# Kernel tuning notes

Measured on AMD Instinct MI355X. Metric: run time of the kernel, lower is better.

## Reference

```python
import jax, jax.numpy as jnp
import numpy as np

NEG_SLOPE = 0.2  # PyG GATConv default negative_slope
HEADS1, HID = 8, 256


def gat_conv(x, src, dst, W, att_src, att_dst, bias, heads, out_ch):
    """PyG-style GATConv: project, per-edge attention, segment softmax over dst, scatter-add."""
    N = x.shape[0]
    h = (x @ W.T).reshape(N, heads, out_ch)                 # [N,H,C]
    a_s = jnp.einsum('nhc,hc->nh', h, att_src)              # [N,H]
    a_d = jnp.einsum('nhc,hc->nh', h, att_dst)
    e = jax.nn.leaky_relu(a_s[src] + a_d[dst], NEG_SLOPE)   # [E,H]
    m = jax.ops.segment_max(e, dst, num_segments=N)         # stable softmax per dst node
    ex = jnp.exp(e - m[dst])
    denom = jax.ops.segment_sum(ex, dst, num_segments=N)
    alpha = ex / (denom[dst] + 1e-16)                       # [E,H]
    out = jax.ops.segment_sum(alpha[:, :, None] * h[src], dst, num_segments=N)  # [N,H,C]
    return out.reshape(N, heads * out_ch) + bias


def setup_inputs() -> dict:
    key = jax.random.key(0)
    ks = jax.random.split(key, 20)
    Nc, Ncol, E = 4000, 16000, 100000
    nf, cf, gain, hid, H, emb = 64, 128, 2, HID, HEADS1, 128
    s = 0.05
    return {
        'constraints_state': jax.random.normal(ks[0], (Nc, nf), jnp.float32),
        'columns_state':     jax.random.normal(ks[1], (Ncol, cf), jnp.float32),
        'edges':             jax.random.randint(ks[2], (2, E), 0, Nc + Ncol, jnp.int64),
        'W_node': jax.random.normal(ks[3], (hid, nf * gain), jnp.float32) * s,
        'b_node': jnp.zeros((hid,), jnp.float32),
        'W_col':  jax.random.normal(ks[4], (hid, cf * gain), jnp.float32) * s,
        'b_col':  jnp.zeros((hid,), jnp.float32),
        'W1':       jax.random.normal(ks[5], (H * hid, hid), jnp.float32) * s,
        'att_src1': jax.random.normal(ks[6], (H, hid), jnp.float32) * s,
        'att_dst1': jax.random.normal(ks[7], (H, hid), jnp.float32) * s,
        'b1':       jnp.zeros((H * hid,), jnp.float32),
        'W2':       jax.random.normal(ks[8], (hid, H * hid), jnp.float32) * s,
        'att_src2': jax.random.normal(ks[9], (1, hid), jnp.float32) * s,
        'att_dst2': jax.random.normal(ks[10], (1, hid), jnp.float32) * s,
        'b2':       jnp.zeros((hid,), jnp.float32),
        'W_out': jax.random.normal(ks[11], (emb, hid), jnp.float32) * s,
        'b_out': jnp.zeros((emb,), jnp.float32),
    }


def reference(constraints_state, columns_state, edges,
              W_node, b_node, W_col, b_col,
              W1, att_src1, att_dst1, b1,
              W2, att_src2, att_dst2, b2,
              W_out, b_out):
    gain = 2
    x_n = jnp.tile(constraints_state, (1, gain))
    x_c = jnp.tile(columns_state, (1, gain))
    h_n = jax.nn.relu(x_n @ W_node.T + b_node)
    h_c = jax.nn.relu(x_c @ W_col.T + b_col)
    x = jnp.concatenate([h_n, h_c], axis=0)                 # [N, hid]
    N = x.shape[0]
    loops = jnp.arange(N)
    # conv1: edges as given (+ self-loops, PyG default)
    src1 = jnp.concatenate([edges[0], loops])
    dst1 = jnp.concatenate([edges[1], loops])
    x = jax.nn.relu(gat_conv(x, src1, dst1, W1, att_src1, att_dst1, b1, HEADS1, HID))
    # conv2: flipped edges (+ self-loops), 1 head
    src2 = jnp.concatenate([edges[1], loops])
    dst2 = jnp.concatenate([edges[0], loops])
    x = jax.nn.relu(gat_conv(x, src2, dst2, W2, att_src2, att_dst2, b2, 1, HID))
    logits = x[-columns_state.shape[0]:] @ W_out.T + b_out  # [Ncol, embed_dim]
    return logits
```

## Files before the change

kernel.cpp:

```cpp
#include <hip/hip_runtime.h>


#define NEG_SLOPE 0.2f

typedef __attribute__((ext_vector_type(8))) short bf16x8;
typedef __attribute__((ext_vector_type(4))) float f32x4;

__device__ __forceinline__ float bf2f(unsigned short u) {
  return __uint_as_float(((unsigned)u) << 16);
}
__device__ __forceinline__ unsigned short f2bf(float f) {
  unsigned u = __float_as_uint(f);
  u += 0x7fffu + ((u >> 16) & 1u);
  return (unsigned short)(u >> 16);
}

__device__ __forceinline__ void async_copy16(const void* g, void* l) {
  __builtin_amdgcn_global_load_lds(
      (const __attribute__((address_space(1))) unsigned int*)g,
      (__attribute__((address_space(3))) unsigned int*)l, 16, 0, 0);
}

__global__ void prep(const float* __restrict__ Wn, const float* __restrict__ Wc,
                     const float* __restrict__ W1, const float* __restrict__ W2,
                     const float* __restrict__ Wout,
                     const float* __restrict__ cons, const float* __restrict__ cols,
                     const float* __restrict__ att_s1, const float* __restrict__ att_d1,
                     unsigned short* __restrict__ Wn_b, unsigned short* __restrict__ Wc_b,
                     unsigned short* __restrict__ W1b, unsigned short* __restrict__ W2b,
                     unsigned short* __restrict__ Woutb,
                     unsigned short* __restrict__ consb, unsigned short* __restrict__ colsb,
                     float* __restrict__ v_s1, float* __restrict__ v_d1,
                     int n_cons, int n_cols) {
  const int S0 = 256 * 64;
  const int S1 = 256 * 128;
  const int S2 = 2048 * 256;
  const int S3 = 256 * 2048;
  const int S4 = 128 * 256;
  const int S5 = 2048;
  int total = S0 + S1 + S2 + S3 + S4 + n_cons + n_cols + S5;
  for (int idx = blockIdx.x * 256 + threadIdx.x; idx < total; idx += gridDim.x * 256) {
    int i = idx;
    if (i < S0) { int o = i >> 6, j = i & 63;
      Wn_b[i] = f2bf(Wn[o * 128 + j] + Wn[o * 128 + 64 + j]); continue; }
    i -= S0;
    if (i < S1) { int o = i >> 7, j = i & 127;
      Wc_b[i] = f2bf(Wc[o * 256 + j] + Wc[o * 256 + 128 + j]); continue; }
    i -= S1;
    if (i < S2) { W1b[i] = f2bf(W1[i]); continue; }
    i -= S2;
    if (i < S3) { W2b[i] = f2bf(W2[i]); continue; }
    i -= S3;
    if (i < S4) { Woutb[i] = f2bf(Wout[i]); continue; }
    i -= S4;
    if (i < n_cons) { consb[i] = f2bf(cons[i]); continue; }
    i -= n_cons;
    if (i < n_cols) { colsb[i] = f2bf(cols[i]); continue; }
    i -= n_cols;
    {
      int h = i >> 8, k = i & 255;
      const float* Wrow = W1 + (size_t)h * 256 * 256 + k;
      const float* as = att_s1 + h * 256;
      const float* ad = att_d1 + h * 256;
      float s = 0.f, d = 0.f;
      for (int c = 0; c < 256; ++c) {
        float w = Wrow[(size_t)c * 256];
        s += as[c] * w;
        d += ad[c] * w;
      }
      v_s1[i] = s; v_d1[i] = d;
    }
  }
}

__global__ __launch_bounds__(256) void a1_dots(const unsigned short* __restrict__ xb,
                                               const float* __restrict__ v_s,
                                               const float* __restrict__ v_d,
                                               float* __restrict__ a_s,
                                               float* __restrict__ a_d, int N) {
  __shared__ float vs[2048], vd[2048];
  for (int i = threadIdx.x; i < 2048; i += 256) { vs[i] = v_s[i]; vd[i] = v_d[i]; }
  __syncthreads();
  int n = blockIdx.x * 256 + threadIdx.x;
  if (n >= N) return;
  const unsigned short* row = xb + (size_t)n * 256;
  float s[8] = {}, d[8] = {};
  for (int c = 0; c < 256; c += 8) {
    bf16x8 xv = *(const bf16x8*)(row + c);
    float xf[8];
#pragma unroll
    for (int i = 0; i < 8; ++i) xf[i] = bf2f(((const unsigned short*)&xv)[i]);
#pragma unroll
    for (int h = 0; h < 8; ++h)
#pragma unroll
      for (int i = 0; i < 8; ++i) {
        s[h] += xf[i] * vs[h * 256 + c + i];
        d[h] += xf[i] * vd[h * 256 + c + i];
      }
  }
#pragma unroll
  for (int h = 0; h < 8; ++h) { a_s[n * 8 + h] = s[h]; a_d[n * 8 + h] = d[h]; }
}

__global__ __launch_bounds__(256) void a2_dots(const unsigned short* __restrict__ h2,
                                               const float* __restrict__ att_s,
                                               const float* __restrict__ att_d,
                                               float* __restrict__ a_s,
                                               float* __restrict__ a_d, int N) {
  __shared__ float ss[256], sd[256];
  if (threadIdx.x < 256) {
    ss[threadIdx.x] = att_s[threadIdx.x];
    sd[threadIdx.x] = att_d[threadIdx.x];
  }
  __syncthreads();
  int n = blockIdx.x * 256 + threadIdx.x;
  if (n >= N) return;
  const unsigned short* row = h2 + (size_t)n * 256;
  float s = 0.f, d = 0.f;
  for (int c = 0; c < 256; c += 8) {
    bf16x8 xv = *(const bf16x8*)(row + c);
#pragma unroll
    for (int i = 0; i < 8; ++i) {
      float hv = bf2f(((const unsigned short*)&xv)[i]);
      s += hv * ss[c + i];
      d += hv * sd[c + i];
    }
  }
  a_s[n] = s;
  a_d[n] = d;
}

template <bool C_BF16, bool BIAS, bool RELU, bool BDIAG>
__global__ __launch_bounds__(512) void gemm_mfma_bt(const unsigned short* __restrict__ A,
                                                    const unsigned short* __restrict__ W,
                                                    const float* __restrict__ bias,
                                                    void* __restrict__ Cv,
                                                    int M, int K, int Nout, int lda) {
  __shared__ short smem[2 * 128 * 64];
  short* sA = smem;
  short* sB = smem + 128 * 64;
  float* Cf = (float*)Cv;
  unsigned short* Cb = (unsigned short*)Cv;

  const int tid = threadIdx.x;
  const int lane = tid & 63, w = tid >> 6;

  const int gx = gridDim.x;
  const int nwg = gx * gridDim.y;
  int orig = blockIdx.y * gx + blockIdx.x;
  int q = nwg >> 3, r = nwg & 7;
  int xcd = orig & 7, idx = orig >> 3;
  int wg = (xcd < r ? xcd * (q + 1) : r * (q + 1) + (xcd - r) * q) + idx;
  const int m0 = (wg / gx) * 128, n0 = (wg % gx) * 128;

  const int koff = BDIAG ? (n0 >> 8) << 8 : 0;
  const int wm = (w & 3) * 32, wn = (w >> 2) * 64;
  const int fr = lane & 15;
  const int frs = fr & 7;
  const int quad = lane >> 4;

  f32x4 acc[2][4];
#pragma unroll
  for (int i = 0; i < 2; ++i)
#pragma unroll
    for (int j = 0; j < 4; ++j) acc[i][j] = (f32x4){0.f, 0.f, 0.f, 0.f};

  for (int k0 = 0; k0 < K; k0 += 64) {
#pragma unroll
    for (int i = 0; i < 2; ++i) {
      int c = i * 512 + tid;
      int row = c >> 3, kc = c & 7;
      int kcs = kc ^ (row & 7);
      int grow = m0 + row;
      if (grow >= M) grow = M - 1;
      async_copy16(A + (size_t)grow * lda + koff + k0 + kcs * 8, &sA[(i * 512 + w * 64) * 8]);
    }
#pragma unroll
    for (int i = 0; i < 2; ++i) {
      int c = i * 512 + tid;
      int row = c >> 3, kc = c & 7;
      int kcs = kc ^ (row & 7);
      async_copy16(W + (size_t)(n0 + row) * K + k0 + kcs * 8, &sB[(i * 512 + w * 64) * 8]);
    }
    __syncthreads();

#pragma unroll
    for (int ks = 0; ks < 2; ++ks) {
      bf16x8 af[2], bfr[4];
#pragma unroll
      for (int mi = 0; mi < 2; ++mi) {
        int row = wm + mi * 16 + fr;
        af[mi] = *(const bf16x8*)&sA[(row * 8 + ((ks * 4 + quad) ^ frs)) * 8];
      }
#pragma unroll
      for (int ni = 0; ni < 4; ++ni) {
        int row = wn + ni * 16 + fr;
        bfr[ni] = *(const bf16x8*)&sB[(row * 8 + ((ks * 4 + quad) ^ frs)) * 8];
      }
#pragma unroll
      for (int mi = 0; mi < 2; ++mi)
#pragma unroll
        for (int ni = 0; ni < 4; ++ni)
          acc[mi][ni] = __builtin_amdgcn_mfma_f32_16x16x32_bf16(
              af[mi], bfr[ni], acc[mi][ni], 0, 0, 0);
    }
    __syncthreads();
  }

  if (C_BF16) {
    unsigned short* hsh = (unsigned short*)smem;
#pragma unroll
    for (int mi = 0; mi < 2; ++mi)
#pragma unroll
      for (int ni = 0; ni < 4; ++ni) {
        int col = wn + ni * 16 + fr;
        float bv = BIAS ? bias[n0 + col] : 0.f;
        f32x4 v = acc[mi][ni];
#pragma unroll
        for (int r = 0; r < 4; ++r) {
          int row = wm + mi * 16 + quad * 4 + r;
          float x = v[r] + bv;
          if (RELU) x = fmaxf(x, 0.f);
          hsh[row * 128 + (col ^ (((row >> 2) & 3) << 5))] = f2bf(x);
        }
      }
    __syncthreads();
#pragma unroll
    for (int i = 0; i < 4; ++i) {
      int slot = i * 512 + tid;
      int row = slot >> 4, cg = slot & 15;
      int colbase = cg * 8;
      bf16x8 val = *(const bf16x8*)&hsh[row * 128 + (colbase ^ (((row >> 2) & 3) << 5))];
      int grow = m0 + row;
      if (grow < M)
        *(bf16x8*)(Cb + (size_t)grow * Nout + n0 + colbase) = val;
    }
  } else {
#pragma unroll
    for (int mi = 0; mi < 2; ++mi)
#pragma unroll
      for (int ni = 0; ni < 4; ++ni) {
        int col = n0 + wn + ni * 16 + fr;
        float bv = BIAS ? bias[col] : 0.f;
        f32x4 v = acc[mi][ni];
#pragma unroll
        for (int r = 0; r < 4; ++r) {
          int row = m0 + wm + mi * 16 + quad * 4 + r;
          if (row < M) {
            float x = v[r] + bv;
            if (RELU) x = fmaxf(x, 0.f);
            Cf[(size_t)row * Nout + col] = x;
          }
        }
      }
  }
}

__global__ void build_count(const void* __restrict__ edges_raw, int E, int N,
                            int* __restrict__ esrc, int* __restrict__ edst,
                            int* __restrict__ cnt1, int* __restrict__ cnt2, int E1) {
  const long long* p64 = (const long long*)edges_raw;
  const int* p32 = (const int*)edges_raw;
  bool is64 = true;
#pragma unroll
  for (int i = 0; i < 8; ++i) {
    long long v = p64[i];
    if (v < 0 || v >= N) is64 = false;
  }
  int idx = blockIdx.x * 256 + threadIdx.x;
  if (idx >= E1) return;
  int s, d;
  if (idx < E) {
    if (is64) { s = (int)p64[idx]; d = (int)p64[E + idx]; }
    else      { s = p32[idx];      d = p32[E + idx]; }
  } else {
    s = d = idx - E;
  }
  esrc[idx] = s;
  edst[idx] = d;
  atomicAdd(&cnt1[d], 1);
  atomicAdd(&cnt2[s], 1);
}

__device__ __forceinline__ void scan_one(const int* __restrict__ cnt,
                                         int* __restrict__ indptr,
                                         int* __restrict__ cur, int N, int* buf) {
  int t = threadIdx.x, lane = t & 63, w = t >> 6;
  int running = 0;
  for (int base = 0; base < N; base += 1024) {
    int v = (base + t < N) ? cnt[base + t] : 0;
    int incl = v;
#pragma unroll
    for (int off = 1; off < 64; off <<= 1) {
      int y = __shfl_up(incl, off);
      if (lane >= off) incl += y;
    }
    if (lane == 63) buf[w] = incl;
    __syncthreads();
    if (t < 16) {
      int x = buf[t];
#pragma unroll
      for (int off = 1; off < 16; off <<= 1) {
        int y = __shfl_up(x, off);
        if (t >= off) x += y;
      }
      buf[t] = x;
    }
    __syncthreads();
    int woff = w ? buf[w - 1] : 0;
    int tot = buf[15];
    if (base + t < N) {
      int excl = running + woff + incl - v;
      indptr[base + t] = excl;
      cur[base + t] = excl;
    }
    running += tot;
    __syncthreads();
  }
  if (t == 0) indptr[N] = running;
  __syncthreads();
}

__global__ __launch_bounds__(1024) void scan2_kernel(const int* cnt1, int* indptr1, int* cur1,
                                                     const int* cnt2, int* indptr2, int* cur2,
                                                     int N) {
  __shared__ int buf[16];
  scan_one(cnt1, indptr1, cur1, N, buf);
  scan_one(cnt2, indptr2, cur2, N, buf);
}

__global__ void scatter_edges(const int* __restrict__ esrc, const int* __restrict__ edst,
                              int* __restrict__ cur1, int* __restrict__ cur2,
                              int* __restrict__ nbr1, int* __restrict__ nbr2, int E1) {
  int e = blockIdx.x * 256 + threadIdx.x;
  if (e >= E1) return;
  int s = esrc[e], d = edst[e];
  int p1 = atomicAdd(&cur1[d], 1);
  nbr1[p1] = s;
  int p2 = atomicAdd(&cur2[s], 1);
  nbr2[p2] = d;
}

__global__ __launch_bounds__(256) void alpha1_kernel(const float* __restrict__ a_s,
                                                     const float* __restrict__ a_d,
                                                     const int* __restrict__ indptr,
                                                     const int* __restrict__ nbr,
                                                     float* __restrict__ alpha, int N) {
  int n = blockIdx.x * 256 + threadIdx.x;
  if (n >= N) return;
  int start = indptr[n], end = indptr[n + 1];
  float ad[8];
  *(float4*)&ad[0] = *(const float4*)&a_d[n * 8];
  *(float4*)&ad[4] = *(const float4*)&a_d[n * 8 + 4];
  float m[8], ssum[8];
#pragma unroll
  for (int h = 0; h < 8; ++h) { m[h] = -1e30f; ssum[h] = 0.f; }
  for (int p = start; p < end; ++p) {
    int s = nbr[p];
    float as[8];
    *(float4*)&as[0] = *(const float4*)&a_s[s * 8];
    *(float4*)&as[4] = *(const float4*)&a_s[s * 8 + 4];
#pragma unroll
    for (int h = 0; h < 8; ++h) {
      float e = as[h] + ad[h];
      e = e > 0.f ? e : NEG_SLOPE * e;
      float nm = fmaxf(m[h], e);
      ssum[h] = ssum[h] * __expf(m[h] - nm) + __expf(e - nm);
      m[h] = nm;
    }
  }
  float inv[8];
#pragma unroll
  for (int h = 0; h < 8; ++h) inv[h] = 1.f / (ssum[h] + 1e-16f);
  for (int p = start; p < end; ++p) {
    int s = nbr[p];
    float as[8];
    *(float4*)&as[0] = *(const float4*)&a_s[s * 8];
    *(float4*)&as[4] = *(const float4*)&a_s[s * 8 + 4];
    float av[8];
#pragma unroll
    for (int h = 0; h < 8; ++h) {
      float e = as[h] + ad[h];
      e = e > 0.f ? e : NEG_SLOPE * e;
      av[h] = __expf(e - m[h]) * inv[h];
    }
    *(float4*)&alpha[(size_t)p * 8] = *(const float4*)&av[0];
    *(float4*)&alpha[(size_t)p * 8 + 4] = *(const float4*)&av[4];
  }
}

__global__ __launch_bounds__(256) void agg1_kernel(const unsigned short* __restrict__ xb,
                                                   const float* __restrict__ alpha,
                                                   const int* __restrict__ indptr,
                                                   const int* __restrict__ nbr,
                                                   unsigned short* __restrict__ agg,
                                                   int N) {
  __shared__ float al_sh[4][64 * 8];
  const int w = threadIdx.x >> 6, lane = threadIdx.x & 63;
  const int dst = blockIdx.x * 4 + w;
  if (dst >= N) return;
  const int start = indptr[dst];
  const int deg = indptr[dst + 1] - start;
  const int c0 = lane * 4;

  float acc[8][4];
#pragma unroll
  for (int h = 0; h < 8; ++h)
#pragma unroll
    for (int i = 0; i < 4; ++i) acc[h][i] = 0.f;

  for (int base = 0; base < deg; base += 64) {
    int cnt = min(64, deg - base);
    int s = 0;
    if (lane < cnt) {
      int slot = start + base + lane;
      s = nbr[slot];
      f32x4 a0 = *(const f32x4*)&alpha[(size_t)slot * 8];
      f32x4 a1 = *(const f32x4*)&alpha[(size_t)slot * 8 + 4];
      *(f32x4*)&al_sh[w][lane * 8] = a0;
      *(f32x4*)&al_sh[w][lane * 8 + 4] = a1;
    }
    __builtin_amdgcn_wave_barrier();
    for (int j = 0; j < cnt; ++j) {
      int sj = __shfl(s, j);
      f32x4 alo = *(const f32x4*)&al_sh[w][j * 8];
      f32x4 ahi = *(const f32x4*)&al_sh[w][j * 8 + 4];
      ushort4 xv = *(const ushort4*)(xb + (size_t)sj * 256 + c0);
      float x0 = bf2f(xv.x), x1 = bf2f(xv.y), x2 = bf2f(xv.z), x3 = bf2f(xv.w);
#pragma unroll
      for (int h = 0; h < 4; ++h) {
        acc[h][0] += alo[h] * x0; acc[h][1] += alo[h] * x1;
        acc[h][2] += alo[h] * x2; acc[h][3] += alo[h] * x3;
      }
#pragma unroll
      for (int h = 0; h < 4; ++h) {
        acc[h + 4][0] += ahi[h] * x0; acc[h + 4][1] += ahi[h] * x1;
        acc[h + 4][2] += ahi[h] * x2; acc[h + 4][3] += ahi[h] * x3;
      }
    }
    __builtin_amdgcn_wave_barrier();
  }

  unsigned short* op = agg + (size_t)dst * 2048;
#pragma unroll
  for (int h = 0; h < 8; ++h) {
    unsigned short ov[4];
#pragma unroll
    for (int i = 0; i < 4; ++i) ov[i] = f2bf(acc[h][i]);
    *((ushort4*)(op + h * 256 + c0)) = *((const ushort4*)ov);
  }
}

__global__ __launch_bounds__(256) void agg2_fused(const unsigned short* __restrict__ h2,
                                                  const float* __restrict__ a_s,
                                                  const float* __restrict__ a_d,
                                                  const int* __restrict__ indptr,
                                                  const int* __restrict__ nbr,
                                                  const float* __restrict__ b2,
                                                  unsigned short* __restrict__ x3,
                                                  int Nc, int Ncol) {
  const int w = threadIdx.x >> 6, lane = threadIdx.x & 63;
  const int i0 = blockIdx.x * 4 + w;
  if (i0 >= Ncol) return;
  const int dst = Nc + i0;
  const int start = indptr[dst];
  const int deg = indptr[dst + 1] - start;
  const float ad = a_d[dst];
  float run_m = -1e30f, run_s = 0.f;
  float acc[4] = {0.f, 0.f, 0.f, 0.f};
  const int c0 = lane * 4;

  for (int base = 0; base < deg; base += 64) {
    int cnt = min(64, deg - base);
    float ev = -1e30f;
    int s = 0;
    if (lane < cnt) {
      s = nbr[start + base + lane];
      float e = a_s[s] + ad;
      ev = e > 0.f ? e : NEG_SLOPE * e;
    }
    float cm = ev;
#pragma unroll
    for (int off = 32; off; off >>= 1) cm = fmaxf(cm, __shfl_xor(cm, off));
    float nm = fmaxf(run_m, cm);
    float sc = __expf(run_m - nm);
    float e = (lane < cnt) ? __expf(ev - nm) : 0.f;
    float cs = e;
#pragma unroll
    for (int off = 32; off; off >>= 1) cs += __shfl_xor(cs, off);
    run_s = run_s * sc + cs;
    run_m = nm;
#pragma unroll
    for (int i = 0; i < 4; ++i) acc[i] *= sc;
    for (int j = 0; j < cnt; ++j) {
      int sj = __shfl(s, j);
      float al = __shfl(e, j);
      ushort4 hv = *(const ushort4*)(h2 + (size_t)sj * 256 + c0);
      acc[0] += al * bf2f(hv.x);
      acc[1] += al * bf2f(hv.y);
      acc[2] += al * bf2f(hv.z);
      acc[3] += al * bf2f(hv.w);
    }
  }

  float inv = 1.f / (run_s + 1e-16f);
  float4 bv = *(const float4*)&b2[c0];
  unsigned short ov[4];
  ov[0] = f2bf(fmaxf(acc[0] * inv + bv.x, 0.f));
  ov[1] = f2bf(fmaxf(acc[1] * inv + bv.y, 0.f));
  ov[2] = f2bf(fmaxf(acc[2] * inv + bv.z, 0.f));
  ov[3] = f2bf(fmaxf(acc[3] * inv + bv.w, 0.f));
  *((ushort4*)(x3 + (size_t)i0 * 256 + c0)) = *((const ushort4*)ov);
}

extern "C" void kernel_launch(void* const* d_in, const int* in_sizes, int n_in,
                              void* d_out, int out_size, void* d_ws, size_t ws_size,
                              hipStream_t stream) {
  (void)n_in; (void)out_size; (void)ws_size;
  const float* constraints = (const float*)d_in[0];
  const float* columns     = (const float*)d_in[1];
  const void*  edges       = d_in[2];
  const float* W_node = (const float*)d_in[3];
  const float* b_node = (const float*)d_in[4];
  const float* W_col  = (const float*)d_in[5];
  const float* b_col  = (const float*)d_in[6];
  const float* W1       = (const float*)d_in[7];
  const float* att_src1 = (const float*)d_in[8];
  const float* att_dst1 = (const float*)d_in[9];
  const float* b1       = (const float*)d_in[10];
  const float* W2       = (const float*)d_in[11];
  const float* att_src2 = (const float*)d_in[12];
  const float* att_dst2 = (const float*)d_in[13];
  const float* b2       = (const float*)d_in[14];
  const float* W_out    = (const float*)d_in[15];
  const float* b_out    = (const float*)d_in[16];

  const int Nc   = in_sizes[0] / 64;
  const int Ncol = in_sizes[1] / 128;
  const int E    = in_sizes[2] / 2;
  const int N    = Nc + Ncol;
  const int E1   = E + N;

  char* p = (char*)d_ws;
  size_t off = 0;
  auto alloc = [&](size_t nbytes) -> void* {
    void* r = p + off;
    off = (off + nbytes + 255) & ~(size_t)255;
    return r;
  };
  unsigned short* Wn_b  = (unsigned short*)alloc(2ull * 256 * 64);
  unsigned short* Wc_b  = (unsigned short*)alloc(2ull * 256 * 128);
  unsigned short* W1b   = (unsigned short*)alloc(2ull * 2048 * 256);
  unsigned short* W2b   = (unsigned short*)alloc(2ull * 256 * 2048);
  unsigned short* Woutb = (unsigned short*)alloc(2ull * 128 * 256);
  unsigned short* consb = (unsigned short*)alloc(2ull * (size_t)Nc * 64);
  unsigned short* colsb = (unsigned short*)alloc(2ull * (size_t)Ncol * 128);
  unsigned short* xb    = (unsigned short*)alloc(2ull * (size_t)N * 256);
  float* v_s1 = (float*)alloc(sizeof(float) * 8 * 256);
  float* v_d1 = (float*)alloc(sizeof(float) * 8 * 256);
  float* a_s1 = (float*)alloc(sizeof(float) * (size_t)N * 8);
  float* a_d1 = (float*)alloc(sizeof(float) * (size_t)N * 8);
  int* esrc = (int*)alloc(4ull * E1);
  int* edst = (int*)alloc(4ull * E1);
  int* cnt1 = (int*)alloc(4ull * 2 * N);
  int* cnt2 = cnt1 + N;
  int* indptr1 = (int*)alloc(4ull * (N + 1));
  int* cur1    = (int*)alloc(4ull * N);
  int* indptr2 = (int*)alloc(4ull * (N + 1));
  int* cur2    = (int*)alloc(4ull * N);
  int* nbr1 = (int*)alloc(4ull * E1);
  int* nbr2 = (int*)alloc(4ull * E1);
  float* alpha1 = (float*)alloc(sizeof(float) * 8ull * E1);
  unsigned short* agg = (unsigned short*)alloc(2ull * (size_t)N * 2048);
  unsigned short* x2  = (unsigned short*)alloc(2ull * (size_t)N * 2048);
  unsigned short* h2b = (unsigned short*)alloc(2ull * (size_t)N * 256);
  float* a_s2 = (float*)alloc(sizeof(float) * (size_t)N);
  float* a_d2 = (float*)alloc(sizeof(float) * (size_t)N);
  unsigned short* x3 = (unsigned short*)alloc(2ull * (size_t)Ncol * 256);

  hipMemsetAsync(cnt1, 0, 4ull * 2 * N, stream);
  prep<<<1024, 256, 0, stream>>>(W_node, W_col, W1, W2, W_out, constraints, columns,
                                 att_src1, att_dst1,
                                 Wn_b, Wc_b, W1b, W2b, Woutb, consb, colsb,
                                 v_s1, v_d1, Nc * 64, Ncol * 128);

  gemm_mfma_bt<true, true, true, false><<<dim3(2, (Nc + 127) / 128), 512, 0, stream>>>(
      consb, Wn_b, b_node, xb, Nc, 64, 256, 64);
  gemm_mfma_bt<true, true, true, false><<<dim3(2, (Ncol + 127) / 128), 512, 0, stream>>>(
      colsb, Wc_b, b_col, xb + (size_t)Nc * 256, Ncol, 128, 256, 128);

  a1_dots<<<(N + 255) / 256, 256, 0, stream>>>(xb, v_s1, v_d1, a_s1, a_d1, N);

  build_count<<<(E1 + 255) / 256, 256, 0, stream>>>(edges, E, N, esrc, edst, cnt1, cnt2, E1);
  scan2_kernel<<<1, 1024, 0, stream>>>(cnt1, indptr1, cur1, cnt2, indptr2, cur2, N);
  scatter_edges<<<(E1 + 255) / 256, 256, 0, stream>>>(esrc, edst, cur1, cur2, nbr1, nbr2, E1);

  alpha1_kernel<<<(N + 255) / 256, 256, 0, stream>>>(a_s1, a_d1, indptr1, nbr1, alpha1, N);
  agg1_kernel<<<(N + 3) / 4, 256, 0, stream>>>(xb, alpha1, indptr1, nbr1, agg, N);
  gemm_mfma_bt<true, true, true, true><<<dim3(16, (N + 127) / 128), 512, 0, stream>>>(
      agg, W1b, b1, x2, N, 256, 2048, 2048);

  gemm_mfma_bt<true, false, false, false><<<dim3(2, (N + 127) / 128), 512, 0, stream>>>(
      x2, W2b, nullptr, h2b, N, 2048, 256, 2048);
  a2_dots<<<(N + 255) / 256, 256, 0, stream>>>(h2b, att_src2, att_dst2, a_s2, a_d2, N);
  agg2_fused<<<(Ncol + 3) / 4, 256, 0, stream>>>(h2b, a_s2, a_d2, indptr2, nbr2, b2, x3,
                                                 Nc, Ncol);

  gemm_mfma_bt<false, true, false, false><<<dim3(1, (Ncol + 127) / 128), 512, 0, stream>>>(
      x3, Woutb, b_out, (float*)d_out, Ncol, 256, 128, 256);
}
```

Before: 373.6 us.

## Fuse conv1 softmax into aggregation with online softmax; parallelize scans; make XCD swizzle optional

Drops the separate alpha1 kernel and its per-edge alpha buffer. The aggregation kernel now computes attention logits per 64-edge chunk and keeps a running max and sum per head across chunks, rescaling the accumulators when the max changes. The two prefix scans run in two blocks instead of one serial block, and the XCD workgroup remapping in the GEMM is kept only for the large conv1 GEMM. This saves a kernel launch and the alpha write and read, but adds wave reductions and exponentials to each chunk of the aggregation.

```diff
diff --git a/kernel.cpp b/kernel.cpp
--- a/kernel.cpp
+++ b/kernel.cpp
@@ -130,7 +130,7 @@
   a_d[n] = d;
 }
 
-template <bool C_BF16, bool BIAS, bool RELU, bool BDIAG>
+template <bool C_BF16, bool BIAS, bool RELU, bool BDIAG, bool SWZ>
 __global__ __launch_bounds__(512) void gemm_mfma_bt(const unsigned short* __restrict__ A,
                                                     const unsigned short* __restrict__ W,
                                                     const float* __restrict__ bias,
@@ -146,11 +146,14 @@
   const int lane = tid & 63, w = tid >> 6;
 
   const int gx = gridDim.x;
-  const int nwg = gx * gridDim.y;
-  int orig = blockIdx.y * gx + blockIdx.x;
-  int q = nwg >> 3, r = nwg & 7;
-  int xcd = orig & 7, idx = orig >> 3;
-  int wg = (xcd < r ? xcd * (q + 1) : r * (q + 1) + (xcd - r) * q) + idx;
+  int wg = blockIdx.y * gx + blockIdx.x;
+  if (SWZ) {
+    const int nwg = gx * gridDim.y;
+    int orig = wg;
+    int q = nwg >> 3, r = nwg & 7;
+    int xcd = orig & 7, idx = orig >> 3;
+    wg = (xcd < r ? xcd * (q + 1) : r * (q + 1) + (xcd - r) * q) + idx;
+  }
   const int m0 = (wg / gx) * 128, n0 = (wg % gx) * 128;
 
   const int koff = BDIAG ? (n0 >> 8) << 8 : 0;
@@ -325,8 +328,8 @@
                                                      const int* cnt2, int* indptr2, int* cur2,
                                                      int N) {
   __shared__ int buf[16];
-  scan_one(cnt1, indptr1, cur1, N, buf);
-  scan_one(cnt2, indptr2, cur2, N, buf);
+  if (blockIdx.x == 0) scan_one(cnt1, indptr1, cur1, N, buf);
+  else                 scan_one(cnt2, indptr2, cur2, N, buf);
 }
 
 __global__ void scatter_edges(const int* __restrict__ esrc, const int* __restrict__ edst,
@@ -341,60 +344,13 @@
   nbr2[p2] = d;
 }
 
-__global__ __launch_bounds__(256) void alpha1_kernel(const float* __restrict__ a_s,
-                                                     const float* __restrict__ a_d,
-                                                     const int* __restrict__ indptr,
-                                                     const int* __restrict__ nbr,
-                                                     float* __restrict__ alpha, int N) {
-  int n = blockIdx.x * 256 + threadIdx.x;
-  if (n >= N) return;
-  int start = indptr[n], end = indptr[n + 1];
-  float ad[8];
-  *(float4*)&ad[0] = *(const float4*)&a_d[n * 8];
-  *(float4*)&ad[4] = *(const float4*)&a_d[n * 8 + 4];
-  float m[8], ssum[8];
-#pragma unroll
-  for (int h = 0; h < 8; ++h) { m[h] = -1e30f; ssum[h] = 0.f; }
-  for (int p = start; p < end; ++p) {
-    int s = nbr[p];
-    float as[8];
-    *(float4*)&as[0] = *(const float4*)&a_s[s * 8];
-    *(float4*)&as[4] = *(const float4*)&a_s[s * 8 + 4];
-#pragma unroll
-    for (int h = 0; h < 8; ++h) {
-      float e = as[h] + ad[h];
-      e = e > 0.f ? e : NEG_SLOPE * e;
-      float nm = fmaxf(m[h], e);
-      ssum[h] = ssum[h] * __expf(m[h] - nm) + __expf(e - nm);
-      m[h] = nm;
-    }
-  }
-  float inv[8];
-#pragma unroll
-  for (int h = 0; h < 8; ++h) inv[h] = 1.f / (ssum[h] + 1e-16f);
-  for (int p = start; p < end; ++p) {
-    int s = nbr[p];
-    float as[8];
-    *(float4*)&as[0] = *(const float4*)&a_s[s * 8];
-    *(float4*)&as[4] = *(const float4*)&a_s[s * 8 + 4];
-    float av[8];
-#pragma unroll
-    for (int h = 0; h < 8; ++h) {
-      float e = as[h] + ad[h];
-      e = e > 0.f ? e : NEG_SLOPE * e;
-      av[h] = __expf(e - m[h]) * inv[h];
-    }
-    *(float4*)&alpha[(size_t)p * 8] = *(const float4*)&av[0];
-    *(float4*)&alpha[(size_t)p * 8 + 4] = *(const float4*)&av[4];
-  }
-}
-
-__global__ __launch_bounds__(256) void agg1_kernel(const unsigned short* __restrict__ xb,
-                                                   const float* __restrict__ alpha,
-                                                   const int* __restrict__ indptr,
-                                                   const int* __restrict__ nbr,
-                                                   unsigned short* __restrict__ agg,
-                                                   int N) {
+__global__ __launch_bounds__(256) void agg1_fused(const unsigned short* __restrict__ xb,
+                                                  const float* __restrict__ a_s,
+                                                  const float* __restrict__ a_d,
+                                                  const int* __restrict__ indptr,
+                                                  const int* __restrict__ nbr,
+                                                  unsigned short* __restrict__ agg,
+                                                  int N) {
   __shared__ float al_sh[4][64 * 8];
   const int w = threadIdx.x >> 6, lane = threadIdx.x & 63;
   const int dst = blockIdx.x * 4 + w;
@@ -403,6 +359,14 @@
   const int deg = indptr[dst + 1] - start;
   const int c0 = lane * 4;
 
+  float ad[8];
+  *(float4*)&ad[0] = *(const float4*)&a_d[dst * 8];
+  *(float4*)&ad[4] = *(const float4*)&a_d[dst * 8 + 4];
+
+  float run_m[8], run_s[8];
+#pragma unroll
+  for (int h = 0; h < 8; ++h) { run_m[h] = -1e30f; run_s[h] = 0.f; }
+
   float acc[8][4];
 #pragma unroll
   for (int h = 0; h < 8; ++h)
@@ -412,13 +376,41 @@
   for (int base = 0; base < deg; base += 64) {
     int cnt = min(64, deg - base);
     int s = 0;
+    float ev[8];
+#pragma unroll
+    for (int h = 0; h < 8; ++h) ev[h] = -1e30f;
     if (lane < cnt) {
-      int slot = start + base + lane;
-      s = nbr[slot];
-      f32x4 a0 = *(const f32x4*)&alpha[(size_t)slot * 8];
-      f32x4 a1 = *(const f32x4*)&alpha[(size_t)slot * 8 + 4];
-      *(f32x4*)&al_sh[w][lane * 8] = a0;
-      *(f32x4*)&al_sh[w][lane * 8 + 4] = a1;
+      s = nbr[start + base + lane];
+      float as[8];
+      *(float4*)&as[0] = *(const float4*)&a_s[s * 8];
+      *(float4*)&as[4] = *(const float4*)&a_s[s * 8 + 4];
+#pragma unroll
+      for (int h = 0; h < 8; ++h) {
+        float e = as[h] + ad[h];
+        ev[h] = e > 0.f ? e : NEG_SLOPE * e;
+      }
+    }
+    float e8[8];
+#pragma unroll
+    for (int h = 0; h < 8; ++h) {
+      float cm = ev[h];
+#pragma unroll
+      for (int off = 32; off; off >>= 1) cm = fmaxf(cm, __shfl_xor(cm, off));
+      float nm = fmaxf(run_m[h], cm);
+      float sc = __expf(run_m[h] - nm);
+      float e = (lane < cnt) ? __expf(ev[h] - nm) : 0.f;
+      float cs = e;
+#pragma unroll
+      for (int off = 32; off; off >>= 1) cs += __shfl_xor(cs, off);
+      run_s[h] = run_s[h] * sc + cs;
+      run_m[h] = nm;
+#pragma unroll
+      for (int i = 0; i < 4; ++i) acc[h][i] *= sc;
+      e8[h] = e;
+    }
+    if (lane < cnt) {
+#pragma unroll
+      for (int h = 0; h < 8; ++h) al_sh[w][lane * 8 + h] = e8[h];
     }
     __builtin_amdgcn_wave_barrier();
     for (int j = 0; j < cnt; ++j) {
@@ -441,12 +433,16 @@
     __builtin_amdgcn_wave_barrier();
   }
 
+  float inv[8];
+#pragma unroll
+  for (int h = 0; h < 8; ++h) inv[h] = 1.f / (run_s[h] + 1e-16f);
+
   unsigned short* op = agg + (size_t)dst * 2048;
 #pragma unroll
   for (int h = 0; h < 8; ++h) {
     unsigned short ov[4];
 #pragma unroll
-    for (int i = 0; i < 4; ++i) ov[i] = f2bf(acc[h][i]);
+    for (int i = 0; i < 4; ++i) ov[i] = f2bf(acc[h][i] * inv[h]);
     *((ushort4*)(op + h * 256 + c0)) = *((const ushort4*)ov);
   }
 }
@@ -570,7 +566,6 @@
   int* cur2    = (int*)alloc(4ull * N);
   int* nbr1 = (int*)alloc(4ull * E1);
   int* nbr2 = (int*)alloc(4ull * E1);
-  float* alpha1 = (float*)alloc(sizeof(float) * 8ull * E1);
   unsigned short* agg = (unsigned short*)alloc(2ull * (size_t)N * 2048);
   unsigned short* x2  = (unsigned short*)alloc(2ull * (size_t)N * 2048);
   unsigned short* h2b = (unsigned short*)alloc(2ull * (size_t)N * 256);
@@ -584,28 +579,27 @@
                                  Wn_b, Wc_b, W1b, W2b, Woutb, consb, colsb,
                                  v_s1, v_d1, Nc * 64, Ncol * 128);
 
-  gemm_mfma_bt<true, true, true, false><<<dim3(2, (Nc + 127) / 128), 512, 0, stream>>>(
+  gemm_mfma_bt<true, true, true, false, false><<<dim3(2, (Nc + 127) / 128), 512, 0, stream>>>(
       consb, Wn_b, b_node, xb, Nc, 64, 256, 64);
-  gemm_mfma_bt<true, true, true, false><<<dim3(2, (Ncol + 127) / 128), 512, 0, stream>>>(
+  gemm_mfma_bt<true, true, true, false, false><<<dim3(2, (Ncol + 127) / 128), 512, 0, stream>>>(
       colsb, Wc_b, b_col, xb + (size_t)Nc * 256, Ncol, 128, 256, 128);
 
   a1_dots<<<(N + 255) / 256, 256, 0, stream>>>(xb, v_s1, v_d1, a_s1, a_d1, N);
 
   build_count<<<(E1 + 255) / 256, 256, 0, stream>>>(edges, E, N, esrc, edst, cnt1, cnt2, E1);
-  scan2_kernel<<<1, 1024, 0, stream>>>(cnt1, indptr1, cur1, cnt2, indptr2, cur2, N);
+  scan2_kernel<<<2, 1024, 0, stream>>>(cnt1, indptr1, cur1, cnt2, indptr2, cur2, N);
   scatter_edges<<<(E1 + 255) / 256, 256, 0, stream>>>(esrc, edst, cur1, cur2, nbr1, nbr2, E1);
 
-  alpha1_kernel<<<(N + 255) / 256, 256, 0, stream>>>(a_s1, a_d1, indptr1, nbr1, alpha1, N);
-  agg1_kernel<<<(N + 3) / 4, 256, 0, stream>>>(xb, alpha1, indptr1, nbr1, agg, N);
-  gemm_mfma_bt<true, true, true, true><<<dim3(16, (N + 127) / 128), 512, 0, stream>>>(
+  agg1_fused<<<(N + 3) / 4, 256, 0, stream>>>(xb, a_s1, a_d1, indptr1, nbr1, agg, N);
+  gemm_mfma_bt<true, true, true, true, true><<<dim3(16, (N + 127) / 128), 512, 0, stream>>>(
       agg, W1b, b1, x2, N, 256, 2048, 2048);
 
-  gemm_mfma_bt<true, false, false, false><<<dim3(2, (N + 127) / 128), 512, 0, stream>>>(
+  gemm_mfma_bt<true, false, false, false, false><<<dim3(2, (N + 127) / 128), 512, 0, stream>>>(
       x2, W2b, nullptr, h2b, N, 2048, 256, 2048);
   a2_dots<<<(N + 255) / 256, 256, 0, stream>>>(h2b, att_src2, att_dst2, a_s2, a_d2, N);
   agg2_fused<<<(Ncol + 3) / 4, 256, 0, stream>>>(h2b, a_s2, a_d2, indptr2, nbr2, b2, x3,
                                                  Nc, Ncol);
 
-  gemm_mfma_bt<false, true, false, false><<<dim3(1, (Ncol + 127) / 128), 512, 0, stream>>>(
+  gemm_mfma_bt<false, true, false, false, false><<<dim3(1, (Ncol + 127) / 128), 512, 0, stream>>>(
       x3, Woutb, b_out, (float*)d_out, Ncol, 256, 128, 256);
 }
```

Result: faster. 361.9 us (-3.1%).
